# Performance work log

Measured on AMD Instinct MI355X. Metric: run time of the kernel, lower is better.

The kernel has to match this reference:

```python
import jax, jax.numpy as jnp
import numpy as np

N = 4096          # nproteins
IN_F = 512        # in_features
OUT_F = 64        # out_features
ALPHA = 0.2       # leakyrelu slope
EPS = 1e-5        # batchnorm eps
NEG = -9e15       # mask fill value from the original code


def setup_inputs() -> dict:
    key = jax.random.key(0)
    k = jax.random.split(key, 5)
    h = jax.random.normal(k[0], (N, IN_F), dtype=jnp.float32)
    # sparse 0/1 adjacency (avg degree ~20) stored dense, as the module expects
    adj = (jax.random.uniform(k[1], (N, N)) < 0.005).astype(jnp.float32)
    half = IN_F // 2
    # xavier_uniform with gain=1.414 ~ U(-b, b), b = gain*sqrt(6/(fan_in+fan_out))
    b_w = 1.414 * np.sqrt(6.0 / (half + OUT_F))
    W1 = jax.random.uniform(k[2], (half, OUT_F), minval=-b_w, maxval=b_w, dtype=jnp.float32)
    W2 = jax.random.uniform(k[3], (half, OUT_F), minval=-b_w, maxval=b_w, dtype=jnp.float32)
    b_a = 1.414 * np.sqrt(6.0 / (2 * OUT_F + 1))
    a = jax.random.uniform(k[4], (2 * OUT_F, 1), minval=-b_a, maxval=b_a, dtype=jnp.float32)
    gamma = jnp.ones((2 * OUT_F,), dtype=jnp.float32)   # bn2 weight
    beta = jnp.zeros((2 * OUT_F,), dtype=jnp.float32)   # bn2 bias
    return {"h": h, "adj": adj, "W1": W1, "W2": W2, "a": a, "gamma": gamma, "beta": beta}


def _lrelu(x):
    return jnp.where(x > 0, x, ALPHA * x)


def reference(h, adj, W1, W2, a, gamma, beta):
    d = h.shape[1] // 2
    Wh1 = h[:, :d] @ W1          # [N, F]
    Wh2 = h[:, d:] @ W2          # [N, F]

    def prep(Wh):
        s1 = Wh @ a[:OUT_F]      # [N, 1]
        s2 = Wh @ a[OUT_F:]      # [N, 1]
        return _lrelu(s1 + s2.T)  # [N, N]

    e1 = prep(Wh1)
    e2 = prep(Wh2)

    adj2 = adj @ adj                               # 2-hop counts [N, N]
    adj2 = adj2 - jnp.diag(jnp.diag(adj2))         # zero the diagonal

    att1 = jax.nn.softmax(jnp.where(adj > 0, e1, NEG), axis=1)
    h_prime1 = att1 @ Wh1                          # [N, F]
    att2 = jax.nn.softmax(jnp.where(adj2 > 0, e2, NEG), axis=1)
    h_prime2 = att2 @ Wh2                          # [N, F]

    hp = jnp.concatenate([h_prime1, h_prime2], axis=-1)  # [N, 2F]
    # BatchNorm1d (training-mode batch stats, biased variance)
    mean = hp.mean(axis=0)
    var = hp.var(axis=0)
    out = gamma * (hp - mean) / jnp.sqrt(var + EPS) + beta
    return _lrelu(out)  # concat=True branch
```

## Files before the change

kernel.cpp:

```cpp
#include <hip/hip_runtime.h>
#include <hip/hip_bf16.h>

#define NN 4096
#define IN_F 512
#define HALF 256
#define FF 64
#define ALPHA 0.2f
#define EPSV 1e-5f
#define CAP1 128
#define CAP2 1024

typedef unsigned long long u64;
typedef unsigned int u32;
typedef unsigned short u16;
typedef unsigned char u8;

__device__ __forceinline__ float lrelu(float x){ return x > 0.f ? x : ALPHA * x; }

__device__ __forceinline__ float wave_fmax(float v){
    #pragma unroll
    for (int off = 32; off; off >>= 1) v = fmaxf(v, __shfl_xor(v, off, 64));
    return v;
}
__device__ __forceinline__ float wave_fsum(float v){
    #pragma unroll
    for (int off = 32; off; off >>= 1) v += __shfl_xor(v, off, 64);
    return v;
}

__device__ __forceinline__ int build_idx16(u64 bits, int lane, int cap, u16* __restrict__ nbr){
    int pc = __popcll(bits);
    int scan = pc;
    #pragma unroll
    for (int off = 1; off < 64; off <<= 1) {
        int v = __shfl_up(scan, off, 64);
        if (lane >= off) scan += v;
    }
    int total = __shfl(scan, 63, 64);
    int pos = scan - pc;
    while (bits) {
        int b = __builtin_ctzll(bits);
        bits &= bits - 1;
        if (pos < cap) nbr[pos] = (u16)((lane << 6) | b);
        ++pos;
    }
    return total;
}

__global__ __launch_bounds__(256) void pack_kernel(const float* __restrict__ adj,
                                                   u16* __restrict__ pack16) {
    __shared__ u8 nib[1024];
    int i = blockIdx.x;
    int tid = threadIdx.x;
    const float4* row = (const float4*)(adj + (size_t)i * NN);
    float4 v0 = row[tid];
    float4 v1 = row[256 + tid];
    float4 v2 = row[512 + tid];
    float4 v3 = row[768 + tid];
    nib[tid]       = (u8)((v0.x > 0.f) | ((u32)(v0.y > 0.f) << 1) | ((u32)(v0.z > 0.f) << 2) | ((u32)(v0.w > 0.f) << 3));
    nib[256 + tid] = (u8)((v1.x > 0.f) | ((u32)(v1.y > 0.f) << 1) | ((u32)(v1.z > 0.f) << 2) | ((u32)(v1.w > 0.f) << 3));
    nib[512 + tid] = (u8)((v2.x > 0.f) | ((u32)(v2.y > 0.f) << 1) | ((u32)(v2.z > 0.f) << 2) | ((u32)(v2.w > 0.f) << 3));
    nib[768 + tid] = (u8)((v3.x > 0.f) | ((u32)(v3.y > 0.f) << 1) | ((u32)(v3.z > 0.f) << 2) | ((u32)(v3.w > 0.f) << 3));
    __syncthreads();
    u32 x = ((const u32*)nib)[tid];
    u16 wd = (u16)((x & 0xFu) | ((x >> 4) & 0xF0u) | ((x >> 8) & 0xF00u) | ((x >> 12) & 0xF000u));
    pack16[(size_t)i * 256 + tid] = wd;
}

__global__ __launch_bounds__(256) void wh_kernel(const float* __restrict__ h,
                                                 const float* __restrict__ W1,
                                                 const float* __restrict__ W2,
                                                 const float* __restrict__ a,
                                                 float* __restrict__ Wh1,
                                                 float* __restrict__ Wh2,
                                                 float* __restrict__ s11,
                                                 float* __restrict__ s12,
                                                 float* __restrict__ s21,
                                                 float* __restrict__ s22) {
    __shared__ float hs[8 * IN_F];
    int tid = threadIdx.x;
    int r0 = blockIdx.x * 8;
    const float4* hsrc = (const float4*)(h + (size_t)r0 * IN_F);
    float4* hdst = (float4*)hs;
    #pragma unroll
    for (int t = 0; t < 4; ++t) hdst[tid + 256 * t] = hsrc[tid + 256 * t];
    __syncthreads();

    int w = tid >> 6, f = tid & 63;
    int br2 = w >> 1;
    int rbase = (w & 1) * 4;
    const float* W = br2 ? W2 : W1;
    const float4* hw4 = (const float4*)(hs + rbase * IN_F + br2 * HALF);
    float acc0 = 0.f, acc1 = 0.f, acc2 = 0.f, acc3 = 0.f;
    #pragma unroll 4
    for (int k4 = 0; k4 < HALF / 4; ++k4) {
        float4 h0 = hw4[k4];
        float4 h1 = hw4[k4 + IN_F / 4];
        float4 h2 = hw4[k4 + 2 * (IN_F / 4)];
        float4 h3 = hw4[k4 + 3 * (IN_F / 4)];
        int k = k4 << 2;
        float w0 = W[(k + 0) * FF + f];
        float w1 = W[(k + 1) * FF + f];
        float w2 = W[(k + 2) * FF + f];
        float w3 = W[(k + 3) * FF + f];
        acc0 += h0.x * w0 + h0.y * w1 + h0.z * w2 + h0.w * w3;
        acc1 += h1.x * w0 + h1.y * w1 + h1.z * w2 + h1.w * w3;
        acc2 += h2.x * w0 + h2.y * w1 + h2.z * w2 + h2.w * w3;
        acc3 += h3.x * w0 + h3.y * w1 + h3.z * w2 + h3.w * w3;
    }
    float* Wh = br2 ? Wh2 : Wh1;
    int rr = r0 + rbase;
    Wh[(size_t)(rr + 0) * FF + f] = acc0;
    Wh[(size_t)(rr + 1) * FF + f] = acc1;
    Wh[(size_t)(rr + 2) * FF + f] = acc2;
    Wh[(size_t)(rr + 3) * FF + f] = acc3;

    float a1 = a[f], a2 = a[64 + f];
    #pragma unroll
    for (int r = 0; r < 4; ++r) {
        float acc = (r == 0) ? acc0 : (r == 1) ? acc1 : (r == 2) ? acc2 : acc3;
        float v1 = acc * a1, v2 = acc * a2;
        #pragma unroll
        for (int off = 32; off; off >>= 1) {
            v1 += __shfl_down(v1, off, 64);
            v2 += __shfl_down(v2, off, 64);
        }
        if (f == 0) {
            if (br2 == 0) { s11[rr + r] = v1; s12[rr + r] = v2; }
            else          { s21[rr + r] = v1; s22[rr + r] = v2; }
        }
    }
}

__global__ __launch_bounds__(256) void attn_kernel(const u64* __restrict__ packA,
                                                   const float* __restrict__ Wh1,
                                                   const float* __restrict__ Wh2,
                                                   const float* __restrict__ s11,
                                                   const float* __restrict__ s12,
                                                   const float* __restrict__ s21,
                                                   const float* __restrict__ s22,
                                                   float* __restrict__ hp) {
    __shared__ u16   nbr1s[4][CAP1];
    __shared__ u16   nbr2s[4][CAP2];
    __shared__ float evs[4][CAP2];

    int tid = threadIdx.x;
    int w = tid >> 6, lane = tid & 63;
    int i = blockIdx.x * 4 + w;

    u16*   nbr1 = nbr1s[w];
    u16*   nbr2 = nbr2s[w];
    float* ev   = evs[w];

    int t1 = build_idx16(packA[(size_t)i * 64 + lane], lane, CAP1, nbr1);
    int c1 = min(t1, CAP1);

    float out1;
    if (c1 > 0) {
        int c1p = (c1 + 7) & ~7;
        if (lane < c1p - c1) { nbr1[c1 + lane] = 0; }
        float s11i = s11[i];
        float lm = -3.4e38f;
        for (int n = lane; n < c1; n += 64) {
            float e = lrelu(s11i + s12[nbr1[n]]);
            ev[n] = e;
            lm = fmaxf(lm, e);
        }
        float m = wave_fmax(lm);
        float ls = 0.f;
        for (int n = lane; n < c1; n += 64) {
            float p = __expf(ev[n] - m);
            ev[n] = p;
            ls += p;
        }
        float invZ = 1.f / wave_fsum(ls);
        if (lane < c1p - c1) { ev[c1 + lane] = 0.f; }
        float a0 = 0.f, a1 = 0.f, a2 = 0.f, a3 = 0.f;
        for (int n = 0; n < c1p; n += 8) {
            ushort4 nA = *(const ushort4*)&nbr1[n];
            ushort4 nB = *(const ushort4*)&nbr1[n + 4];
            float4  wA = *(const float4*)&ev[n];
            float4  wB = *(const float4*)&ev[n + 4];
            float q0 = Wh1[(int)nA.x * FF + lane];
            float q1 = Wh1[(int)nA.y * FF + lane];
            float q2 = Wh1[(int)nA.z * FF + lane];
            float q3 = Wh1[(int)nA.w * FF + lane];
            float q4 = Wh1[(int)nB.x * FF + lane];
            float q5 = Wh1[(int)nB.y * FF + lane];
            float q6 = Wh1[(int)nB.z * FF + lane];
            float q7 = Wh1[(int)nB.w * FF + lane];
            a0 += wA.x * q0 + wB.x * q4;
            a1 += wA.y * q1 + wB.y * q5;
            a2 += wA.z * q2 + wB.z * q6;
            a3 += wA.w * q3 + wB.w * q7;
        }
        out1 = ((a0 + a1) + (a2 + a3)) * invZ;
    } else {
        float a0 = 0.f, a1 = 0.f, a2 = 0.f, a3 = 0.f;
        for (int n = 0; n < NN; n += 4) {
            a0 += Wh1[(n + 0) * FF + lane];
            a1 += Wh1[(n + 1) * FF + lane];
            a2 += Wh1[(n + 2) * FF + lane];
            a3 += Wh1[(n + 3) * FF + lane];
        }
        out1 = ((a0 + a1) + (a2 + a3)) * (1.f / NN);
    }
    hp[(size_t)i * 128 + lane] = out1;

    u64 w0 = 0, w1 = 0, w2 = 0, w3 = 0;
    {
        int n = 0;
        for (; n + 4 <= c1; n += 4) {
            w0 |= packA[(int)nbr1[n + 0] * 64 + lane];
            w1 |= packA[(int)nbr1[n + 1] * 64 + lane];
            w2 |= packA[(int)nbr1[n + 2] * 64 + lane];
            w3 |= packA[(int)nbr1[n + 3] * 64 + lane];
        }
        for (; n < c1; ++n) w0 |= packA[(int)nbr1[n] * 64 + lane];
    }
    u64 word = (w0 | w1) | (w2 | w3);
    if (lane == (i >> 6)) word &= ~(1ull << (i & 63));

    int t2 = build_idx16(word, lane, CAP2, nbr2);
    int c2 = min(t2, CAP2);

    float out2;
    if (c2 > 0) {
        int c2p = (c2 + 7) & ~7;
        if (lane < c2p - c2) { nbr2[c2 + lane] = 0; }
        float s21i = s21[i];
        float lm = -3.4e38f;
        for (int n = lane; n < c2; n += 64) {
            float e = lrelu(s21i + s22[nbr2[n]]);
            ev[n] = e;
            lm = fmaxf(lm, e);
        }
        float m = wave_fmax(lm);
        float ls = 0.f;
        for (int n = lane; n < c2; n += 64) {
            float p = __expf(ev[n] - m);
            ev[n] = p;
            ls += p;
        }
        float invZ = 1.f / wave_fsum(ls);
        if (lane < c2p - c2) { ev[c2 + lane] = 0.f; }
        float a0 = 0.f, a1 = 0.f, a2 = 0.f, a3 = 0.f;
        for (int n = 0; n < c2p; n += 8) {
            ushort4 nA = *(const ushort4*)&nbr2[n];
            ushort4 nB = *(const ushort4*)&nbr2[n + 4];
            float4  wA = *(const float4*)&ev[n];
            float4  wB = *(const float4*)&ev[n + 4];
            float q0 = Wh2[(int)nA.x * FF + lane];
            float q1 = Wh2[(int)nA.y * FF + lane];
            float q2 = Wh2[(int)nA.z * FF + lane];
            float q3 = Wh2[(int)nA.w * FF + lane];
            float q4 = Wh2[(int)nB.x * FF + lane];
            float q5 = Wh2[(int)nB.y * FF + lane];
            float q6 = Wh2[(int)nB.z * FF + lane];
            float q7 = Wh2[(int)nB.w * FF + lane];
            a0 += wA.x * q0 + wB.x * q4;
            a1 += wA.y * q1 + wB.y * q5;
            a2 += wA.z * q2 + wB.z * q6;
            a3 += wA.w * q3 + wB.w * q7;
        }
        out2 = ((a0 + a1) + (a2 + a3)) * invZ;
    } else {
        float a0 = 0.f, a1 = 0.f, a2 = 0.f, a3 = 0.f;
        for (int n = 0; n < NN; n += 4) {
            a0 += Wh2[(n + 0) * FF + lane];
            a1 += Wh2[(n + 1) * FF + lane];
            a2 += Wh2[(n + 2) * FF + lane];
            a3 += Wh2[(n + 3) * FF + lane];
        }
        out2 = ((a0 + a1) + (a2 + a3)) * (1.f / NN);
    }
    hp[(size_t)i * 128 + 64 + lane] = out2;
}

__global__ __launch_bounds__(256) void stats_kernel(const float* __restrict__ hp,
                                                    float* __restrict__ ps,
                                                    float* __restrict__ pq) {
    __shared__ float ls[128], lq[128];
    int tid = threadIdx.x;
    if (tid < 128) { ls[tid] = 0.f; lq[tid] = 0.f; }
    __syncthreads();
    float s0 = 0, s1 = 0, s2 = 0, s3 = 0, q0 = 0, q1 = 0, q2 = 0, q3 = 0;
    const float4* hp4 = (const float4*)hp;
    for (size_t idx = (size_t)blockIdx.x * 256 + tid; idx < (size_t)NN * 32;
         idx += (size_t)gridDim.x * 256) {
        float4 v = hp4[idx];
        s0 += v.x; q0 += v.x * v.x;
        s1 += v.y; q1 += v.y * v.y;
        s2 += v.z; q2 += v.z * v.z;
        s3 += v.w; q3 += v.w * v.w;
    }
    int cb = (tid & 31) << 2;
    atomicAdd(&ls[cb + 0], s0); atomicAdd(&lq[cb + 0], q0);
    atomicAdd(&ls[cb + 1], s1); atomicAdd(&lq[cb + 1], q1);
    atomicAdd(&ls[cb + 2], s2); atomicAdd(&lq[cb + 2], q2);
    atomicAdd(&ls[cb + 3], s3); atomicAdd(&lq[cb + 3], q3);
    __syncthreads();
    if (tid < 128) {
        ps[(size_t)blockIdx.x * 128 + tid] = ls[tid];
        pq[(size_t)blockIdx.x * 128 + tid] = lq[tid];
    }
}

__global__ __launch_bounds__(256) void normf_kernel(float* __restrict__ hp,
                                                    const float* __restrict__ ps,
                                                    const float* __restrict__ pq,
                                                    const float* __restrict__ gamma,
                                                    const float* __restrict__ beta) {
    __shared__ float csum[256];
    __shared__ float cmean[128], cginv[128];
    int tid = threadIdx.x;
    {
        const float* src = (tid < 128) ? ps : pq;
        int c = tid & 127;
        float s = 0.f;
        #pragma unroll 8
        for (int b = 0; b < 128; ++b) s += src[b * 128 + c];
        csum[tid] = s;
    }
    __syncthreads();
    if (tid < 128) {
        float mean = csum[tid] * (1.f / NN);
        float var = csum[128 + tid] * (1.f / NN) - mean * mean;
        cmean[tid] = mean;
        cginv[tid] = rsqrtf(var + EPSV) * gamma[tid];
    }
    __syncthreads();

    size_t idx = (size_t)blockIdx.x * 256 + tid;
    if (idx < (size_t)NN * 32) {
        int cb = (int)((idx << 2) & 127);
        float4 v = ((const float4*)hp)[idx];
        float r[4] = {v.x, v.y, v.z, v.w};
        #pragma unroll
        for (int t = 0; t < 4; ++t) {
            int c = cb + t;
            r[t] = lrelu((r[t] - cmean[c]) * cginv[c] + beta[c]);
        }
        ((float4*)hp)[idx] = make_float4(r[0], r[1], r[2], r[3]);
    }
}

extern "C" void kernel_launch(void* const* d_in, const int* in_sizes, int n_in,
                              void* d_out, int out_size, void* d_ws, size_t ws_size,
                              hipStream_t stream) {
    const float* h     = (const float*)d_in[0];
    const float* adj   = (const float*)d_in[1];
    const float* W1    = (const float*)d_in[2];
    const float* W2    = (const float*)d_in[3];
    const float* a     = (const float*)d_in[4];
    const float* gamma = (const float*)d_in[5];
    const float* beta  = (const float*)d_in[6];
    float* hp = (float*)d_out;

    u64* packA  = (u64*)d_ws;
    float* Wh1  = (float*)(packA + (size_t)NN * 64);
    float* Wh2  = Wh1 + (size_t)NN * FF;
    float* s11  = Wh2 + (size_t)NN * FF;
    float* s12  = s11 + NN;
    float* s21  = s12 + NN;
    float* s22  = s21 + NN;
    float* ps   = s22 + NN;
    float* pq   = ps + 128 * 128;

    pack_kernel<<<NN, 256, 0, stream>>>(adj, (u16*)packA);
    wh_kernel<<<NN / 8, 256, 0, stream>>>(h, W1, W2, a, Wh1, Wh2, s11, s12, s21, s22);
    attn_kernel<<<NN / 4, 256, 0, stream>>>(packA, Wh1, Wh2, s11, s12, s21, s22, hp);
    stats_kernel<<<128, 256, 0, stream>>>(hp, ps, pq);
    normf_kernel<<<(NN * 32 + 255) / 256, 256, 0, stream>>>(hp, ps, pq, gamma, beta);
}
```

Baseline: 163.2 us.

## Merge pack and Wh kernels, fold BN stats into attention epilogue

```diff
diff --git a/kernel.cpp b/kernel.cpp
--- a/kernel.cpp
+++ b/kernel.cpp
@@ -9,6 +9,7 @@
 #define EPSV 1e-5f
 #define CAP1 128
 #define CAP2 1024
+#define WHB (NN / 8)
 
 typedef unsigned long long u64;
 typedef unsigned int u32;
@@ -47,88 +48,91 @@
     return total;
 }
 
-__global__ __launch_bounds__(256) void pack_kernel(const float* __restrict__ adj,
-                                                   u16* __restrict__ pack16) {
-    __shared__ u8 nib[1024];
-    int i = blockIdx.x;
-    int tid = threadIdx.x;
-    const float4* row = (const float4*)(adj + (size_t)i * NN);
-    float4 v0 = row[tid];
-    float4 v1 = row[256 + tid];
-    float4 v2 = row[512 + tid];
-    float4 v3 = row[768 + tid];
-    nib[tid]       = (u8)((v0.x > 0.f) | ((u32)(v0.y > 0.f) << 1) | ((u32)(v0.z > 0.f) << 2) | ((u32)(v0.w > 0.f) << 3));
-    nib[256 + tid] = (u8)((v1.x > 0.f) | ((u32)(v1.y > 0.f) << 1) | ((u32)(v1.z > 0.f) << 2) | ((u32)(v1.w > 0.f) << 3));
-    nib[512 + tid] = (u8)((v2.x > 0.f) | ((u32)(v2.y > 0.f) << 1) | ((u32)(v2.z > 0.f) << 2) | ((u32)(v2.w > 0.f) << 3));
-    nib[768 + tid] = (u8)((v3.x > 0.f) | ((u32)(v3.y > 0.f) << 1) | ((u32)(v3.z > 0.f) << 2) | ((u32)(v3.w > 0.f) << 3));
-    __syncthreads();
-    u32 x = ((const u32*)nib)[tid];
-    u16 wd = (u16)((x & 0xFu) | ((x >> 4) & 0xF0u) | ((x >> 8) & 0xF00u) | ((x >> 12) & 0xF000u));
-    pack16[(size_t)i * 256 + tid] = wd;
-}
-
-__global__ __launch_bounds__(256) void wh_kernel(const float* __restrict__ h,
-                                                 const float* __restrict__ W1,
-                                                 const float* __restrict__ W2,
-                                                 const float* __restrict__ a,
-                                                 float* __restrict__ Wh1,
-                                                 float* __restrict__ Wh2,
-                                                 float* __restrict__ s11,
-                                                 float* __restrict__ s12,
-                                                 float* __restrict__ s21,
-                                                 float* __restrict__ s22) {
+__global__ __launch_bounds__(256) void packwh_kernel(const float* __restrict__ adj,
+                                                     u16* __restrict__ pack16,
+                                                     const float* __restrict__ h,
+                                                     const float* __restrict__ W1,
+                                                     const float* __restrict__ W2,
+                                                     const float* __restrict__ a,
+                                                     float* __restrict__ Wh1,
+                                                     float* __restrict__ Wh2,
+                                                     float* __restrict__ s11,
+                                                     float* __restrict__ s12,
+                                                     float* __restrict__ s21,
+                                                     float* __restrict__ s22,
+                                                     float* __restrict__ colsum) {
     __shared__ float hs[8 * IN_F];
     int tid = threadIdx.x;
-    int r0 = blockIdx.x * 8;
-    const float4* hsrc = (const float4*)(h + (size_t)r0 * IN_F);
-    float4* hdst = (float4*)hs;
-    #pragma unroll
-    for (int t = 0; t < 4; ++t) hdst[tid + 256 * t] = hsrc[tid + 256 * t];
-    __syncthreads();
-
-    int w = tid >> 6, f = tid & 63;
-    int br2 = w >> 1;
-    int rbase = (w & 1) * 4;
-    const float* W = br2 ? W2 : W1;
-    const float4* hw4 = (const float4*)(hs + rbase * IN_F + br2 * HALF);
-    float acc0 = 0.f, acc1 = 0.f, acc2 = 0.f, acc3 = 0.f;
-    #pragma unroll 4
-    for (int k4 = 0; k4 < HALF / 4; ++k4) {
-        float4 h0 = hw4[k4];
-        float4 h1 = hw4[k4 + IN_F / 4];
-        float4 h2 = hw4[k4 + 2 * (IN_F / 4)];
-        float4 h3 = hw4[k4 + 3 * (IN_F / 4)];
-        int k = k4 << 2;
-        float w0 = W[(k + 0) * FF + f];
-        float w1 = W[(k + 1) * FF + f];
-        float w2 = W[(k + 2) * FF + f];
-        float w3 = W[(k + 3) * FF + f];
-        acc0 += h0.x * w0 + h0.y * w1 + h0.z * w2 + h0.w * w3;
-        acc1 += h1.x * w0 + h1.y * w1 + h1.z * w2 + h1.w * w3;
-        acc2 += h2.x * w0 + h2.y * w1 + h2.z * w2 + h2.w * w3;
-        acc3 += h3.x * w0 + h3.y * w1 + h3.z * w2 + h3.w * w3;
-    }
-    float* Wh = br2 ? Wh2 : Wh1;
-    int rr = r0 + rbase;
-    Wh[(size_t)(rr + 0) * FF + f] = acc0;
-    Wh[(size_t)(rr + 1) * FF + f] = acc1;
-    Wh[(size_t)(rr + 2) * FF + f] = acc2;
-    Wh[(size_t)(rr + 3) * FF + f] = acc3;
-
-    float a1 = a[f], a2 = a[64 + f];
-    #pragma unroll
-    for (int r = 0; r < 4; ++r) {
-        float acc = (r == 0) ? acc0 : (r == 1) ? acc1 : (r == 2) ? acc2 : acc3;
-        float v1 = acc * a1, v2 = acc * a2;
+    if (blockIdx.x < NN) {
+        u8* nib = (u8*)hs;
+        int i = blockIdx.x;
+        const float4* row = (const float4*)(adj + (size_t)i * NN);
+        float4 v0 = row[tid];
+        float4 v1 = row[256 + tid];
+        float4 v2 = row[512 + tid];
+        float4 v3 = row[768 + tid];
+        nib[tid]       = (u8)((v0.x > 0.f) | ((u32)(v0.y > 0.f) << 1) | ((u32)(v0.z > 0.f) << 2) | ((u32)(v0.w > 0.f) << 3));
+        nib[256 + tid] = (u8)((v1.x > 0.f) | ((u32)(v1.y > 0.f) << 1) | ((u32)(v1.z > 0.f) << 2) | ((u32)(v1.w > 0.f) << 3));
+        nib[512 + tid] = (u8)((v2.x > 0.f) | ((u32)(v2.y > 0.f) << 1) | ((u32)(v2.z > 0.f) << 2) | ((u32)(v2.w > 0.f) << 3));
+        nib[768 + tid] = (u8)((v3.x > 0.f) | ((u32)(v3.y > 0.f) << 1) | ((u32)(v3.z > 0.f) << 2) | ((u32)(v3.w > 0.f) << 3));
+        __syncthreads();
+        u32 x = ((const u32*)nib)[tid];
+        u16 wd = (u16)((x & 0xFu) | ((x >> 4) & 0xF0u) | ((x >> 8) & 0xF00u) | ((x >> 12) & 0xF000u));
+        pack16[(size_t)i * 256 + tid] = wd;
+    } else if (blockIdx.x < NN + WHB) {
+        int r0 = (blockIdx.x - NN) * 8;
+        const float4* hsrc = (const float4*)(h + (size_t)r0 * IN_F);
+        float4* hdst = (float4*)hs;
         #pragma unroll
-        for (int off = 32; off; off >>= 1) {
-            v1 += __shfl_down(v1, off, 64);
-            v2 += __shfl_down(v2, off, 64);
-        }
-        if (f == 0) {
-            if (br2 == 0) { s11[rr + r] = v1; s12[rr + r] = v2; }
-            else          { s21[rr + r] = v1; s22[rr + r] = v2; }
-        }
+        for (int t = 0; t < 4; ++t) hdst[tid + 256 * t] = hsrc[tid + 256 * t];
+        __syncthreads();
+
+        int w = tid >> 6, f = tid & 63;
+        int br2 = w >> 1;
+        int rbase = (w & 1) * 4;
+        const float* W = br2 ? W2 : W1;
+        const float4* hw4 = (const float4*)(hs + rbase * IN_F + br2 * HALF);
+        float acc0 = 0.f, acc1 = 0.f, acc2 = 0.f, acc3 = 0.f;
+        #pragma unroll 4
+        for (int k4 = 0; k4 < HALF / 4; ++k4) {
+            float4 h0 = hw4[k4];
+            float4 h1 = hw4[k4 + IN_F / 4];
+            float4 h2 = hw4[k4 + 2 * (IN_F / 4)];
+            float4 h3 = hw4[k4 + 3 * (IN_F / 4)];
+            int k = k4 << 2;
+            float w0 = W[(k + 0) * FF + f];
+            float w1 = W[(k + 1) * FF + f];
+            float w2 = W[(k + 2) * FF + f];
+            float w3 = W[(k + 3) * FF + f];
+            acc0 += h0.x * w0 + h0.y * w1 + h0.z * w2 + h0.w * w3;
+            acc1 += h1.x * w0 + h1.y * w1 + h1.z * w2 + h1.w * w3;
+            acc2 += h2.x * w0 + h2.y * w1 + h2.z * w2 + h2.w * w3;
+            acc3 += h3.x * w0 + h3.y * w1 + h3.z * w2 + h3.w * w3;
+        }
+        float* Wh = br2 ? Wh2 : Wh1;
+        int rr = r0 + rbase;
+        Wh[(size_t)(rr + 0) * FF + f] = acc0;
+        Wh[(size_t)(rr + 1) * FF + f] = acc1;
+        Wh[(size_t)(rr + 2) * FF + f] = acc2;
+        Wh[(size_t)(rr + 3) * FF + f] = acc3;
+
+        float a1 = a[f], a2 = a[64 + f];
+        #pragma unroll
+        for (int r = 0; r < 4; ++r) {
+            float acc = (r == 0) ? acc0 : (r == 1) ? acc1 : (r == 2) ? acc2 : acc3;
+            float v1 = acc * a1, v2 = acc * a2;
+            #pragma unroll
+            for (int off = 32; off; off >>= 1) {
+                v1 += __shfl_down(v1, off, 64);
+                v2 += __shfl_down(v2, off, 64);
+            }
+            if (f == 0) {
+                if (br2 == 0) { s11[rr + r] = v1; s12[rr + r] = v2; }
+                else          { s21[rr + r] = v1; s22[rr + r] = v2; }
+            }
+        }
+    } else {
+        colsum[tid] = 0.f;
     }
 }
 
@@ -139,7 +143,9 @@
                                                    const float* __restrict__ s12,
                                                    const float* __restrict__ s21,
                                                    const float* __restrict__ s22,
-                                                   float* __restrict__ hp) {
+                                                   float* __restrict__ hp,
+                                                   float* __restrict__ colsum,
+                                                   float* __restrict__ colsq) {
     __shared__ u16   nbr1s[4][CAP1];
     __shared__ u16   nbr2s[4][CAP2];
     __shared__ float evs[4][CAP2];
@@ -275,59 +281,37 @@
         out2 = ((a0 + a1) + (a2 + a3)) * (1.f / NN);
     }
     hp[(size_t)i * 128 + 64 + lane] = out2;
-}
-
-__global__ __launch_bounds__(256) void stats_kernel(const float* __restrict__ hp,
-                                                    float* __restrict__ ps,
-                                                    float* __restrict__ pq) {
-    __shared__ float ls[128], lq[128];
-    int tid = threadIdx.x;
-    if (tid < 128) { ls[tid] = 0.f; lq[tid] = 0.f; }
-    __syncthreads();
-    float s0 = 0, s1 = 0, s2 = 0, s3 = 0, q0 = 0, q1 = 0, q2 = 0, q3 = 0;
-    const float4* hp4 = (const float4*)hp;
-    for (size_t idx = (size_t)blockIdx.x * 256 + tid; idx < (size_t)NN * 32;
-         idx += (size_t)gridDim.x * 256) {
-        float4 v = hp4[idx];
-        s0 += v.x; q0 += v.x * v.x;
-        s1 += v.y; q1 += v.y * v.y;
-        s2 += v.z; q2 += v.z * v.z;
-        s3 += v.w; q3 += v.w * v.w;
-    }
-    int cb = (tid & 31) << 2;
-    atomicAdd(&ls[cb + 0], s0); atomicAdd(&lq[cb + 0], q0);
-    atomicAdd(&ls[cb + 1], s1); atomicAdd(&lq[cb + 1], q1);
-    atomicAdd(&ls[cb + 2], s2); atomicAdd(&lq[cb + 2], q2);
-    atomicAdd(&ls[cb + 3], s3); atomicAdd(&lq[cb + 3], q3);
+
+    ev[lane]       = out1;
+    ev[64 + lane]  = out1 * out1;
+    ev[128 + lane] = out2;
+    ev[192 + lane] = out2 * out2;
     __syncthreads();
     if (tid < 128) {
-        ps[(size_t)blockIdx.x * 128 + tid] = ls[tid];
-        pq[(size_t)blockIdx.x * 128 + tid] = lq[tid];
+        int base = (tid < 64) ? 0 : 64;
+        int c = tid & 63;
+        float s = evs[0][base * 2 + c]      + evs[1][base * 2 + c]
+                + evs[2][base * 2 + c]      + evs[3][base * 2 + c];
+        float q = evs[0][base * 2 + 64 + c] + evs[1][base * 2 + 64 + c]
+                + evs[2][base * 2 + 64 + c] + evs[3][base * 2 + 64 + c];
+        atomicAdd(&colsum[base + c], s);
+        atomicAdd(&colsq[base + c], q);
     }
 }
 
 __global__ __launch_bounds__(256) void normf_kernel(float* __restrict__ hp,
-                                                    const float* __restrict__ ps,
-                                                    const float* __restrict__ pq,
+                                                    const float* __restrict__ colsum,
+                                                    const float* __restrict__ colsq,
                                                     const float* __restrict__ gamma,
                                                     const float* __restrict__ beta) {
-    __shared__ float csum[256];
-    __shared__ float cmean[128], cginv[128];
+    __shared__ float cmean[128], cginv[128], cbeta[128];
     int tid = threadIdx.x;
-    {
-        const float* src = (tid < 128) ? ps : pq;
-        int c = tid & 127;
-        float s = 0.f;
-        #pragma unroll 8
-        for (int b = 0; b < 128; ++b) s += src[b * 128 + c];
-        csum[tid] = s;
-    }
-    __syncthreads();
     if (tid < 128) {
-        float mean = csum[tid] * (1.f / NN);
-        float var = csum[128 + tid] * (1.f / NN) - mean * mean;
+        float mean = colsum[tid] * (1.f / NN);
+        float var = colsq[tid] * (1.f / NN) - mean * mean;
         cmean[tid] = mean;
         cginv[tid] = rsqrtf(var + EPSV) * gamma[tid];
+        cbeta[tid] = beta[tid];
     }
     __syncthreads();
 
@@ -339,7 +323,7 @@
         #pragma unroll
         for (int t = 0; t < 4; ++t) {
             int c = cb + t;
-            r[t] = lrelu((r[t] - cmean[c]) * cginv[c] + beta[c]);
+            r[t] = lrelu((r[t] - cmean[c]) * cginv[c] + cbeta[c]);
         }
         ((float4*)hp)[idx] = make_float4(r[0], r[1], r[2], r[3]);
     }
@@ -364,12 +348,12 @@
     float* s12  = s11 + NN;
     float* s21  = s12 + NN;
     float* s22  = s21 + NN;
-    float* ps   = s22 + NN;
-    float* pq   = ps + 128 * 128;
-
-    pack_kernel<<<NN, 256, 0, stream>>>(adj, (u16*)packA);
-    wh_kernel<<<NN / 8, 256, 0, stream>>>(h, W1, W2, a, Wh1, Wh2, s11, s12, s21, s22);
-    attn_kernel<<<NN / 4, 256, 0, stream>>>(packA, Wh1, Wh2, s11, s12, s21, s22, hp);
-    stats_kernel<<<128, 256, 0, stream>>>(hp, ps, pq);
-    normf_kernel<<<(NN * 32 + 255) / 256, 256, 0, stream>>>(hp, ps, pq, gamma, beta);
-}
+    float* colsum = s22 + NN;
+    float* colsq  = colsum + 128;
+
+    packwh_kernel<<<NN + WHB + 1, 256, 0, stream>>>(adj, (u16*)packA, h, W1, W2, a,
+                                                    Wh1, Wh2, s11, s12, s21, s22, colsum);
+    attn_kernel<<<NN / 4, 256, 0, stream>>>(packA, Wh1, Wh2, s11, s12, s21, s22,
+                                            hp, colsum, colsq);
+    normf_kernel<<<(NN * 32 + 255) / 256, 256, 0, stream>>>(hp, colsum, colsq, gamma, beta);
+}
```

New measurement: 175.4 us. +7.4%, slower.
